# Performance work log

Hardware: AMD Instinct MI355X
Metric: run time of the kernel (lower is better)

The kernel has to match this reference:

```python
import jax, jax.numpy as jnp
import numpy as np

A = 4096       # padded atoms
M = 64         # max neighbors
DIM_Q = 64     # descriptor dim
H = 128        # hidden neurons
NUM_TYPES = 8
BOX_L = 30.0   # cubic cell length (Angstrom-ish)


def setup_inputs() -> dict:
    key = jax.random.key(0)
    ks = jax.random.split(key, 10)
    descriptors = jax.random.normal(ks[0], (A, DIM_Q), dtype=jnp.float32)
    gradients = jax.random.normal(ks[1], (A, M, 3, DIM_Q), dtype=jnp.float32) * 0.1
    grad_index = jax.random.randint(ks[2], (A, M), 0, A)
    positions = jax.random.uniform(ks[3], (A, 3), dtype=jnp.float32) * BOX_L
    Z = jax.random.randint(ks[4], (A,), 0, NUM_TYPES)
    box = BOX_L * jnp.eye(3, dtype=jnp.float32)
    atom_mask = jnp.ones((A,), dtype=jnp.float32)
    neighbor_mask = (jax.random.uniform(ks[5], (A, M)) < 0.9).astype(jnp.float32)
    # learned parameters (glorot-ish scale)
    W0 = jax.random.normal(ks[6], (NUM_TYPES, DIM_Q, H), dtype=jnp.float32) * (2.0 / (DIM_Q + H)) ** 0.5
    b0 = jnp.zeros((NUM_TYPES, H), dtype=jnp.float32)
    W1 = jax.random.normal(ks[7], (NUM_TYPES, H), dtype=jnp.float32) * (2.0 / (H + 1)) ** 0.5
    b1 = jnp.zeros((), dtype=jnp.float32)
    return {"descriptors": descriptors, "gradients": gradients, "grad_index": grad_index,
            "positions": positions, "Z": Z, "box": box, "atom_mask": atom_mask,
            "neighbor_mask": neighbor_mask, "W0": W0, "b0": b0, "W1": W1, "b1": b1}


def _neighbor_displacements(positions, box, grad_index):
    # minimum-image displacements r_j - r_i for each padded neighbor slot
    dr = positions[grad_index] - positions[:, None, :]          # [A, M, 3]
    inv_box = jnp.linalg.inv(box)
    frac = dr @ inv_box
    frac = frac - jnp.round(frac)
    dr = frac @ box
    rij = jnp.sqrt(jnp.sum(dr * dr, axis=-1))                   # [A, M] distances
    return dr, rij


def reference(descriptors, gradients, grad_index, positions, Z, box, atom_mask, neighbor_mask, W0, b0, W1, b1):
    # per-atom type-gathered weights (deterministic MoE routing by atom type)
    W0_t = W0[Z]                                                # [A, dim_q, H]
    b0_t = b0[Z]                                                # [A, H]
    W1_t = W1[Z]                                                # [A, H]
    # batched small MLP
    h = jnp.einsum('nd,ndh->nh', descriptors, W0_t) + b0_t
    h = jnp.tanh(h)
    h = h * atom_mask[:, None]                                  # [A, H]
    # chain-rule forces dU_i/dR_j
    dtanh = 1.0 - jnp.square(h)
    de_da = dtanh * W1_t                                        # [A, H]
    de_dq = jnp.einsum('nh,nqh->nq', de_da, W0_t)               # [A, dim_q]
    forces = jnp.einsum('nq,nmcq->nmc', de_dq, gradients)       # [A, M, 3]
    forces = forces * neighbor_mask[:, :, None]
    # dipole: -sum_ij |r_ij|^2 * forces
    _, rij = _neighbor_displacements(positions, box, grad_index)
    rij2 = jnp.square(rij) * neighbor_mask                      # [A, M]
    dipole = -jnp.sum(rij2[:, :, None] * forces, axis=(0, 1))   # [3]
    return dipole
```

## Files before the change

kernel.cpp:

```cpp
#include <hip/hip_runtime.h>

#define A_ 4096
#define M_ 64
#define Q_ 64
#define H_ 128

__global__ __launch_bounds__(256, 4) void tnep_fused(
    const float* __restrict__ desc,
    const float* __restrict__ grad,
    const int*   __restrict__ gidx,
    const float* __restrict__ pos,
    const int*   __restrict__ Zt,
    const float* __restrict__ box,
    const float* __restrict__ amask,
    const float* __restrict__ nmask,
    const float* __restrict__ W0,
    const float* __restrict__ b0,
    const float* __restrict__ W1,
    float* __restrict__ partials)
{
    __shared__ __align__(16) float desc_s[Q_];
    __shared__ __align__(16) float dedq_s[Q_];
    __shared__ float coef_s[M_];
    __shared__ float psumF[8 * 132];
    __shared__ __align__(16) float deda_s[H_];
    __shared__ float psumB[Q_ * 33];
    __shared__ float red[3][256];

    const int n = blockIdx.x;
    const int t = threadIdx.x;

    const float4* gbase = (const float4*)(grad + (size_t)n * (M_ * 3 * Q_));
    float4 gpre[12];
    #pragma unroll
    for (int i = 0; i < 12; ++i) gpre[i] = gbase[i * 256 + t];

    const int z = Zt[n];

    const float4* W0z4 = (const float4*)(W0 + (size_t)z * (Q_ * H_));
    float4 w0r[8];
    #pragma unroll
    for (int k = 0; k < 8; ++k) w0r[k] = W0z4[t + 256 * k];

    if (t < 16) ((float4*)desc_s)[t] = ((const float4*)(desc + n * Q_))[t];

    if (t >= 64 && t < 128) {
        int m = t - 64;
        float b00 = box[0], b01 = box[1], b02 = box[2];
        float b10 = box[3], b11 = box[4], b12 = box[5];
        float b20 = box[6], b21 = box[7], b22 = box[8];
        float c00 =   b11 * b22 - b12 * b21;
        float c01 = -(b10 * b22 - b12 * b20);
        float c02 =   b10 * b21 - b11 * b20;
        float det = b00 * c00 + b01 * c01 + b02 * c02;
        float id  = 1.0f / det;
        float i00 = c00 * id;
        float i10 = c01 * id;
        float i20 = c02 * id;
        float i01 = -(b01 * b22 - b02 * b21) * id;
        float i11 =  (b00 * b22 - b02 * b20) * id;
        float i21 = -(b00 * b21 - b01 * b20) * id;
        float i02 =  (b01 * b12 - b02 * b11) * id;
        float i12 = -(b00 * b12 - b02 * b10) * id;
        float i22 =  (b00 * b11 - b01 * b10) * id;

        int j = gidx[n * M_ + m];
        float dx = pos[j * 3 + 0] - pos[n * 3 + 0];
        float dy = pos[j * 3 + 1] - pos[n * 3 + 1];
        float dz = pos[j * 3 + 2] - pos[n * 3 + 2];
        float fx = dx * i00 + dy * i10 + dz * i20;
        float fy = dx * i01 + dy * i11 + dz * i21;
        float fz = dx * i02 + dy * i12 + dz * i22;
        fx -= rintf(fx); fy -= rintf(fy); fz -= rintf(fz);
        float rx = fx * b00 + fy * b10 + fz * b20;
        float ry = fx * b01 + fy * b11 + fz * b21;
        float rz = fx * b02 + fy * b12 + fz * b22;
        float nm = nmask[n * M_ + m];
        coef_s[m] = -((rx * rx + ry * ry + rz * rz) * nm) * nm;
    }
    __syncthreads();

    {
        const int g = t >> 5;
        const int hbase = (t & 31) * 4;
        float fx = 0.f, fy = 0.f, fz = 0.f, fw = 0.f;
        #pragma unroll
        for (int k = 0; k < 8; ++k) {
            float d = desc_s[g + 8 * k];
            float4 w = w0r[k];
            fx += d * w.x; fy += d * w.y; fz += d * w.z; fw += d * w.w;
        }
        psumF[g * 132 + hbase + 0] = fx;
        psumF[g * 132 + hbase + 1] = fy;
        psumF[g * 132 + hbase + 2] = fz;
        psumF[g * 132 + hbase + 3] = fw;
    }
    __syncthreads();

    if (t < H_) {
        float pre = b0[z * H_ + t];
        #pragma unroll
        for (int g = 0; g < 8; ++g) pre += psumF[g * 132 + t];
        float am = amask[n];
        float hv = tanhf(pre) * am;
        deda_s[t] = (1.0f - hv * hv) * W1[z * H_ + t];
    }
    __syncthreads();

    {
        float4 dd = ((const float4*)deda_s)[t & 31];
        #pragma unroll
        for (int k = 0; k < 8; ++k) {
            int q = (t >> 5) + 8 * k;
            float4 w = w0r[k];
            psumB[q * 33 + (t & 31)] =
                w.x * dd.x + w.y * dd.y + w.z * dd.z + w.w * dd.w;
        }
    }
    __syncthreads();

    if (t < Q_) {
        float s = 0.0f;
        #pragma unroll
        for (int v = 0; v < 32; ++v) s += psumB[t * 33 + v];
        dedq_s[t] = s;
    }
    __syncthreads();

    float a0 = 0.f, a1 = 0.f, a2 = 0.f;
    const float4* dq4 = (const float4*)dedq_s;
    #pragma unroll
    for (int i = 0; i < 12; ++i) {
        int idx = i * 256 + t;
        int m   = idx / 48;
        int rc  = idx - m * 48;
        int c   = rc >> 4;
        int q4  = rc & 15;
        float4 g = gpre[i];
        float4 d = dq4[q4];
        float  p = (g.x * d.x + g.y * d.y + g.z * d.z + g.w * d.w) * coef_s[m];
        a0 += (c == 0) ? p : 0.0f;
        a1 += (c == 1) ? p : 0.0f;
        a2 += (c == 2) ? p : 0.0f;
    }
    red[0][t] = a0; red[1][t] = a1; red[2][t] = a2;
    __syncthreads();

    #pragma unroll
    for (int off = 128; off > 0; off >>= 1) {
        if (t < off) {
            red[0][t] += red[0][t + off];
            red[1][t] += red[1][t + off];
            red[2][t] += red[2][t + off];
        }
        __syncthreads();
    }
    if (t < 3) partials[t * A_ + n] = red[t][0];
}

__global__ __launch_bounds__(1024) void tnep_reduce(
    const float* __restrict__ partials, float* __restrict__ out)
{
    __shared__ float sb0[1024], sb1[1024], sb2[1024];
    const int t = threadIdx.x;
    const float4* p4 = (const float4*)partials;
    float4 a = p4[t];
    float4 b = p4[1024 + t];
    float4 c = p4[2048 + t];
    sb0[t] = (a.x + a.y) + (a.z + a.w);
    sb1[t] = (b.x + b.y) + (b.z + b.w);
    sb2[t] = (c.x + c.y) + (c.z + c.w);
    __syncthreads();
    #pragma unroll
    for (int off = 512; off > 0; off >>= 1) {
        if (t < off) {
            sb0[t] += sb0[t + off];
            sb1[t] += sb1[t + off];
            sb2[t] += sb2[t + off];
        }
        __syncthreads();
    }
    if (t == 0) { out[0] = sb0[0]; out[1] = sb1[0]; out[2] = sb2[0]; }
}

extern "C" void kernel_launch(void* const* d_in, const int* in_sizes, int n_in,
                              void* d_out, int out_size, void* d_ws, size_t ws_size,
                              hipStream_t stream) {
    const float* desc  = (const float*)d_in[0];
    const float* grad  = (const float*)d_in[1];
    const int*   gidx  = (const int*)  d_in[2];
    const float* pos   = (const float*)d_in[3];
    const int*   Zt    = (const int*)  d_in[4];
    const float* box   = (const float*)d_in[5];
    const float* amask = (const float*)d_in[6];
    const float* nmask = (const float*)d_in[7];
    const float* W0    = (const float*)d_in[8];
    const float* b0    = (const float*)d_in[9];
    const float* W1    = (const float*)d_in[10];

    float* partials = (float*)d_ws;
    float* out      = (float*)d_out;

    tnep_fused<<<A_, 256, 0, stream>>>(desc, grad, gidx, pos, Zt, box,
                                       amask, nmask, W0, b0, W1, partials);
    tnep_reduce<<<1, 1024, 0, stream>>>(partials, out);
}
```

Measured before the change: 41.92 us.

## Fuse final reduction into main kernel via last-block atomic counter and wave shuffles

Replaces the shared-memory tree reduction per block with wavefront shuffle reductions plus a small cross-wave combine. It also removes the separate reduction kernel launch: each block atomically increments a counter, and the last block to finish sums all partials and writes the output. A memset of the counter is added before the launch. This saves one kernel launch and several barriers, at the cost of an atomic and threadfences per block and a serialized tail on the last block.

```diff
diff --git a/kernel.cpp b/kernel.cpp
--- a/kernel.cpp
+++ b/kernel.cpp
@@ -4,6 +4,7 @@
 #define M_ 64
 #define Q_ 64
 #define H_ 128
+
 
 __global__ __launch_bounds__(256, 4) void tnep_fused(
     const float* __restrict__ desc,
@@ -17,7 +18,9 @@
     const float* __restrict__ W0,
     const float* __restrict__ b0,
     const float* __restrict__ W1,
-    float* __restrict__ partials)
+    float* __restrict__ partials,
+    int*   __restrict__ counter,
+    float* __restrict__ out)
 {
     __shared__ __align__(16) float desc_s[Q_];
     __shared__ __align__(16) float dedq_s[Q_];
@@ -25,7 +28,9 @@
     __shared__ float psumF[8 * 132];
     __shared__ __align__(16) float deda_s[H_];
     __shared__ float psumB[Q_ * 33];
-    __shared__ float red[3][256];
+    __shared__ float wred[3][4];
+    __shared__ float fred[3][256];
+    __shared__ int   last_s;
 
     const int n = blockIdx.x;
     const int t = threadIdx.x;
@@ -143,44 +148,58 @@
         a1 += (c == 1) ? p : 0.0f;
         a2 += (c == 2) ? p : 0.0f;
     }
-    red[0][t] = a0; red[1][t] = a1; red[2][t] = a2;
-    __syncthreads();
-
-    #pragma unroll
-    for (int off = 128; off > 0; off >>= 1) {
-        if (t < off) {
-            red[0][t] += red[0][t + off];
-            red[1][t] += red[1][t + off];
-            red[2][t] += red[2][t + off];
-        }
+
+    #pragma unroll
+    for (int off = 32; off > 0; off >>= 1) {
+        a0 += __shfl_down(a0, off);
+        a1 += __shfl_down(a1, off);
+        a2 += __shfl_down(a2, off);
+    }
+    if ((t & 63) == 0) {
+        int w = t >> 6;
+        wred[0][w] = a0; wred[1][w] = a1; wred[2][w] = a2;
+    }
+    __syncthreads();
+
+    if (t == 0) {
+        float s0 = (wred[0][0] + wred[0][1]) + (wred[0][2] + wred[0][3]);
+        float s1 = (wred[1][0] + wred[1][1]) + (wred[1][2] + wred[1][3]);
+        float s2 = (wred[2][0] + wred[2][1]) + (wred[2][2] + wred[2][3]);
+        partials[n]          = s0;
+        partials[A_ + n]     = s1;
+        partials[2 * A_ + n] = s2;
+        __threadfence();
+        int old = atomicAdd(counter, 1);
+        last_s = (old == A_ - 1) ? 1 : 0;
+    }
+    __syncthreads();
+
+    if (last_s) {
+        __threadfence();
+        const float4* p0 = (const float4*)(partials);
+        const float4* p1 = (const float4*)(partials + A_);
+        const float4* p2 = (const float4*)(partials + 2 * A_);
+        float s0 = 0.f, s1 = 0.f, s2 = 0.f;
+        #pragma unroll
+        for (int k = 0; k < 4; ++k) {
+            int i = k * 256 + t;
+            float4 a = p0[i]; s0 += (a.x + a.y) + (a.z + a.w);
+            float4 b = p1[i]; s1 += (b.x + b.y) + (b.z + b.w);
+            float4 c = p2[i]; s2 += (c.x + c.y) + (c.z + c.w);
+        }
+        fred[0][t] = s0; fred[1][t] = s1; fred[2][t] = s2;
         __syncthreads();
-    }
-    if (t < 3) partials[t * A_ + n] = red[t][0];
-}
-
-__global__ __launch_bounds__(1024) void tnep_reduce(
-    const float* __restrict__ partials, float* __restrict__ out)
-{
-    __shared__ float sb0[1024], sb1[1024], sb2[1024];
-    const int t = threadIdx.x;
-    const float4* p4 = (const float4*)partials;
-    float4 a = p4[t];
-    float4 b = p4[1024 + t];
-    float4 c = p4[2048 + t];
-    sb0[t] = (a.x + a.y) + (a.z + a.w);
-    sb1[t] = (b.x + b.y) + (b.z + b.w);
-    sb2[t] = (c.x + c.y) + (c.z + c.w);
-    __syncthreads();
-    #pragma unroll
-    for (int off = 512; off > 0; off >>= 1) {
-        if (t < off) {
-            sb0[t] += sb0[t + off];
-            sb1[t] += sb1[t + off];
-            sb2[t] += sb2[t + off];
-        }
-        __syncthreads();
-    }
-    if (t == 0) { out[0] = sb0[0]; out[1] = sb1[0]; out[2] = sb2[0]; }
+        #pragma unroll
+        for (int off = 128; off > 0; off >>= 1) {
+            if (t < off) {
+                fred[0][t] += fred[0][t + off];
+                fred[1][t] += fred[1][t + off];
+                fred[2][t] += fred[2][t + off];
+            }
+            __syncthreads();
+        }
+        if (t == 0) { out[0] = fred[0][0]; out[1] = fred[1][0]; out[2] = fred[2][0]; }
+    }
 }
 
 extern "C" void kernel_launch(void* const* d_in, const int* in_sizes, int n_in,
@@ -199,9 +218,11 @@
     const float* W1    = (const float*)d_in[10];
 
     float* partials = (float*)d_ws;
+    int*   counter  = (int*)((float*)d_ws + 3 * A_);
     float* out      = (float*)d_out;
 
+    hipMemsetAsync(counter, 0, sizeof(int), stream);
     tnep_fused<<<A_, 256, 0, stream>>>(desc, grad, gidx, pos, Zt, box,
-                                       amask, nmask, W0, b0, W1, partials);
-    tnep_reduce<<<1, 1024, 0, stream>>>(partials, out);
+                                       amask, nmask, W0, b0, W1,
+                                       partials, counter, out);
 }
```

After: 151.3 us. +261.0%, slower.
